# Performance work log

Hardware: AMD Instinct MI355X
Metric: run time of the kernel (lower is better)

## Reference

```python
import jax, jax.numpy as jnp
import numpy as np


def setup_inputs() -> dict:
    key = jax.random.key(0)
    k1, k2 = jax.random.split(key)
    x = jax.random.normal(k1, (32, 3, 512, 512), dtype=jnp.float32)
    p = jax.random.uniform(k2, (32, 4), dtype=jnp.float32)
    return {"x": x, "p": p}


def _reflect(coord, size):
    # PyTorch grid_sample reflection padding, align_corners=False:
    # reflect about borders at -0.5 and size-0.5 (span = size), then clip.
    span = float(size)
    c = jnp.abs(coord + 0.5)
    flips = jnp.floor(c / span)
    extra = c - flips * span
    c = jnp.where(jnp.mod(flips, 2.0) == 0.0, extra, span - extra) - 0.5
    return jnp.clip(c, 0.0, size - 1.0)


def _bilinear_sample(img, ix, iy, W, H):
    # img: [C,H,W]; ix,iy: [H,W] pixel-space coords already reflected into [0,size-1]
    ix0f = jnp.floor(ix)
    iy0f = jnp.floor(iy)
    fx = ix - ix0f
    fy = iy - iy0f
    x0 = jnp.clip(ix0f.astype(jnp.int32), 0, W - 1)
    x1 = jnp.clip(ix0f.astype(jnp.int32) + 1, 0, W - 1)
    y0 = jnp.clip(iy0f.astype(jnp.int32), 0, H - 1)
    y1 = jnp.clip(iy0f.astype(jnp.int32) + 1, 0, H - 1)
    v00 = img[:, y0, x0]  # [C,H,W]
    v01 = img[:, y0, x1]
    v10 = img[:, y1, x0]
    v11 = img[:, y1, x1]
    return (v00 * (1.0 - fx) * (1.0 - fy)
            + v01 * fx * (1.0 - fy)
            + v10 * (1.0 - fx) * fy
            + v11 * fx * fy)


def reference(x, p):
    B, C, H, W = x.shape
    tx, ty, th, ts = p[:, 0], p[:, 1], p[:, 2], p[:, 3]
    c, s = jnp.cos(th), jnp.sin(th)
    # affine_grid base coords, align_corners=False: centers of pixels in [-1,1]
    xs = (jnp.arange(W, dtype=x.dtype) + 0.5) * (2.0 / W) - 1.0  # [W]
    ys = (jnp.arange(H, dtype=x.dtype) + 0.5) * (2.0 / H) - 1.0  # [H]
    a = (ts * c)[:, None, None]
    b = (-ts * s)[:, None, None]
    d = (ts * s)[:, None, None]
    e = (ts * c)[:, None, None]
    gx = a * xs[None, None, :] + b * ys[None, :, None] + tx[:, None, None]  # [B,H,W]
    gy = d * xs[None, None, :] + e * ys[None, :, None] + ty[:, None, None]  # [B,H,W]
    # unnormalize to pixel space (align_corners=False)
    ix = ((gx + 1.0) * W - 1.0) * 0.5
    iy = ((gy + 1.0) * H - 1.0) * 0.5
    ix = _reflect(ix, W)
    iy = _reflect(iy, H)
    out = jax.vmap(lambda img, jx, jy: _bilinear_sample(img, jx, jy, W, H))(x, ix, iy)
    return out
```

## Files before the change

kernel.cpp:

```cpp
#include <hip/hip_runtime.h>


#define B_ 32
#define C_ 3
#define H_ 512
#define W_ 512
#define TILE 32
#define LSTRIDE 60
#define MAXROWS 55
#define SMEMW (MAXROWS * LSTRIDE + 64)

typedef float f32x4 __attribute__((ext_vector_type(4)));

__device__ __forceinline__ float reflect512(float coord) {
    const float c = fabsf(coord + 0.5f);
    const float m = c - floorf(c * (1.0f / 1024.0f)) * 1024.0f;
    const float t = 512.0f - fabsf(m - 512.0f);
    return fminf(fmaxf(t - 0.5f, 0.0f), 511.0f);
}

__global__ __launch_bounds__(256, 8)
void st_kernel(const float* __restrict__ x, const float* __restrict__ p,
               float* __restrict__ out) {
    __shared__ float smem[SMEMW];

    const int tid = threadIdx.x;

    const int bid = blockIdx.x;
    const int wid = (bid & 7) * 1024 + (bid >> 3);
    const int b   = wid >> 8;
    const int til = wid & 255;
    const int tlx = til & 15;
    const int tly = til >> 4;

    const float tx = p[b * 4 + 0];
    const float ty = p[b * 4 + 1];
    const float th = p[b * 4 + 2];
    const float ts = p[b * 4 + 3];
    const float cth = __cosf(th), sth = __sinf(th);
    const float a  =  ts * cth;
    const float bb = -ts * sth;
    const float d  =  ts * sth;

    const float xs_c = ((float)(tlx * TILE) + 16.0f) * (2.0f / W_) - 1.0f;
    const float ys_c = ((float)(tly * TILE) + 16.0f) * (2.0f / H_) - 1.0f;
    const float gxc = a * xs_c + bb * ys_c + tx;
    const float gyc = d * xs_c + a  * ys_c + ty;
    const float rcx = reflect512(((gxc + 1.0f) * W_ - 1.0f) * 0.5f);
    const float rcy = reflect512(((gyc + 1.0f) * H_ - 1.0f) * 0.5f);
    const float ext = 16.0f * (fabsf(a) + fabsf(bb)) + 3.0f;

    int bx0 = max((int)floorf(rcx - ext), 0) & ~3;
    const int xhi = min((int)ceilf(rcx + ext) + 1, W_);
    int nw4 = (xhi - bx0 + 3) >> 2;
    nw4 = min(min(nw4, 15), (W_ - bx0) >> 2);

    int by0 = max((int)floorf(rcy - ext), 0);
    const int yhi = min((int)ceilf(rcy + ext) + 1, H_);
    const int nrows = min(yhi - by0, MAXROWS);

    const size_t plane = (size_t)H_ * W_;
    const float* img = x + (size_t)b * C_ * plane;
    const int c4 = tid & 15;
    const int r0 = tid >> 4;
    const int ccl = min(c4, max(nw4 - 1, 0)) * 4;
    const float* gp0 = img + (size_t)by0 * W_ + bx0;

    f32x4 vr[4];
    #pragma unroll
    for (int i = 0; i < 4; ++i) {
        const int rr = min(r0 + i * 16, nrows - 1);
        vr[i] = *reinterpret_cast<const f32x4*>(gp0 + (size_t)rr * W_ + ccl);
    }

    const int lr   = tid >> 3;
    const int lc   = (tid & 7) * 4;
    const int row  = tly * TILE + lr;
    const int col0 = tlx * TILE + lc;

    const float ysn = ((float)row  + 0.5f) * (2.0f / H_) - 1.0f;
    const float xsn = ((float)col0 + 0.5f) * (2.0f / W_) - 1.0f;
    float ix = ((a * xsn + bb * ysn + tx + 1.0f) * W_ - 1.0f) * 0.5f;
    float iy = ((d * xsn + a  * ysn + ty + 1.0f) * H_ - 1.0f) * 0.5f;

    const int koff = by0 * LSTRIDE + bx0;
    int   idx4[4];
    float fx_[4], fy_[4];
    #pragma unroll
    for (int k = 0; k < 4; ++k) {
        const float rx  = reflect512(ix);
        const float ry  = reflect512(iy);
        const float x0f = floorf(rx);
        const float y0f = floorf(ry);
        fx_[k] = rx - x0f;
        fy_[k] = ry - y0f;
        idx4[k] = (int)y0f * LSTRIDE + (int)x0f - koff;
        ix += a;
        iy += d;
    }

    #pragma unroll
    for (int i = 0; i < 4; ++i) {
        const int r = r0 + i * 16;
        if (r < nrows && c4 < nw4)
            *reinterpret_cast<f32x4*>(&smem[r * LSTRIDE + c4 * 4]) = vr[i];
    }
    if (nw4 < 15) {
        #pragma unroll
        for (int i = 0; i < 4; ++i) {
            const int r = r0 + i * 16;
            if (r < nrows && c4 == nw4)
                *reinterpret_cast<f32x4*>(&smem[r * LSTRIDE + c4 * 4]) = (f32x4)(0.0f);
        }
    }
    if (tid < 16)
        *reinterpret_cast<f32x4*>(&smem[nrows * LSTRIDE + tid * 4]) = (f32x4)(0.0f);

    float* outp = out + (size_t)b * C_ * plane + (size_t)row * W_ + col0;

    #pragma unroll
    for (int ch = 0; ch < C_; ++ch) {
        __syncthreads();

        float acc[4];
        #pragma unroll
        for (int k = 0; k < 4; ++k) {
            const float fx = fx_[k], fy = fy_[k];
            const float ox = 1.0f - fx, oy = 1.0f - fy;
            const float* s = &smem[idx4[k]];
            acc[k] = s[0] * (ox * oy) + s[1] * (fx * oy)
                   + s[LSTRIDE] * (ox * fy) + s[LSTRIDE + 1] * (fx * fy);
        }
        const f32x4 v = {acc[0], acc[1], acc[2], acc[3]};
        *reinterpret_cast<f32x4*>(outp + (size_t)ch * plane) = v;

        if (ch < C_ - 1) {
            const float* gp = img + (size_t)(ch + 1) * plane
                                  + (size_t)by0 * W_ + bx0;
            #pragma unroll
            for (int i = 0; i < 4; ++i) {
                const int rr = min(r0 + i * 16, nrows - 1);
                vr[i] = *reinterpret_cast<const f32x4*>(gp + (size_t)rr * W_ + ccl);
            }
            __syncthreads();
            #pragma unroll
            for (int i = 0; i < 4; ++i) {
                const int r = r0 + i * 16;
                if (r < nrows && c4 < nw4)
                    *reinterpret_cast<f32x4*>(&smem[r * LSTRIDE + c4 * 4]) = vr[i];
            }
        }
    }
}

extern "C" void kernel_launch(void* const* d_in, const int* in_sizes, int n_in,
                              void* d_out, int out_size, void* d_ws, size_t ws_size,
                              hipStream_t stream) {
    const float* x = (const float*)d_in[0];
    const float* p = (const float*)d_in[1];
    float* out = (float*)d_out;

    dim3 block(256, 1, 1);
    dim3 grid((W_ / TILE) * (H_ / TILE) * B_, 1, 1);
    st_kernel<<<grid, block, 0, stream>>>(x, p, out);
}
```

Before: 179.7 us.

## Give each wavefront its own 16x16 sub-tile window and drop block barriers

Splits the 32x32 output tile into four 16x16 sub-tiles, one per wavefront, each staging its own smaller source window in a private LDS region. Because only one wavefront reads and writes its window, all __syncthreads calls are removed, and the next channel's global loads are issued before the current channel's interpolation so they overlap with compute. The cost is more overlapping halo loads across wavefronts, more registers for eight prefetched vectors, and reliance on wavefront lockstep for LDS ordering with no explicit barrier. Large rotations or scales may exceed the smaller window and get clamped.

```diff
diff --git a/kernel.cpp b/kernel.cpp
--- a/kernel.cpp
+++ b/kernel.cpp
@@ -6,9 +6,10 @@
 #define H_ 512
 #define W_ 512
 #define TILE 32
-#define LSTRIDE 60
-#define MAXROWS 55
-#define SMEMW (MAXROWS * LSTRIDE + 64)
+#define PTILE 16
+#define LSTRIDE 40
+#define WROWS 32
+#define WWORDS (WROWS * LSTRIDE)
 
 typedef float f32x4 __attribute__((ext_vector_type(4)));
 
@@ -22,9 +23,11 @@
 __global__ __launch_bounds__(256, 8)
 void st_kernel(const float* __restrict__ x, const float* __restrict__ p,
                float* __restrict__ out) {
-    __shared__ float smem[SMEMW];
+    __shared__ float smem[4 * WWORDS];
 
-    const int tid = threadIdx.x;
+    const int tid  = threadIdx.x;
+    const int wv   = tid >> 6;
+    const int lane = tid & 63;
 
     const int bid = blockIdx.x;
     const int wid = (bid & 7) * 1024 + (bid >> 3);
@@ -42,41 +45,59 @@
     const float bb = -ts * sth;
     const float d  =  ts * sth;
 
-    const float xs_c = ((float)(tlx * TILE) + 16.0f) * (2.0f / W_) - 1.0f;
-    const float ys_c = ((float)(tly * TILE) + 16.0f) * (2.0f / H_) - 1.0f;
+    const int porow = tly * TILE + (wv >> 1) * PTILE;
+    const int pocol = tlx * TILE + (wv & 1) * PTILE;
+
+    const float xs_c = ((float)pocol + 8.0f) * (2.0f / W_) - 1.0f;
+    const float ys_c = ((float)porow + 8.0f) * (2.0f / H_) - 1.0f;
     const float gxc = a * xs_c + bb * ys_c + tx;
     const float gyc = d * xs_c + a  * ys_c + ty;
     const float rcx = reflect512(((gxc + 1.0f) * W_ - 1.0f) * 0.5f);
     const float rcy = reflect512(((gyc + 1.0f) * H_ - 1.0f) * 0.5f);
-    const float ext = 16.0f * (fabsf(a) + fabsf(bb)) + 3.0f;
+    const float ext = 8.0f * (fabsf(a) + fabsf(bb)) + 3.0f;
 
     int bx0 = max((int)floorf(rcx - ext), 0) & ~3;
     const int xhi = min((int)ceilf(rcx + ext) + 1, W_);
     int nw4 = (xhi - bx0 + 3) >> 2;
-    nw4 = min(min(nw4, 15), (W_ - bx0) >> 2);
+    nw4 = min(min(nw4, 9), (W_ - bx0) >> 2);
 
     int by0 = max((int)floorf(rcy - ext), 0);
     const int yhi = min((int)ceilf(rcy + ext) + 1, H_);
-    const int nrows = min(yhi - by0, MAXROWS);
+    const int nrows = min(yhi - by0, WROWS - 1);
 
     const size_t plane = (size_t)H_ * W_;
     const float* img = x + (size_t)b * C_ * plane;
-    const int c4 = tid & 15;
-    const int r0 = tid >> 4;
-    const int ccl = min(c4, max(nw4 - 1, 0)) * 4;
-    const float* gp0 = img + (size_t)by0 * W_ + bx0;
+    const size_t goff = (size_t)by0 * W_ + bx0;
 
-    f32x4 vr[4];
-    #pragma unroll
-    for (int i = 0; i < 4; ++i) {
-        const int rr = min(r0 + i * 16, nrows - 1);
-        vr[i] = *reinterpret_cast<const f32x4*>(gp0 + (size_t)rr * W_ + ccl);
-    }
+    float* wbase = &smem[wv * WWORDS];
+    const int slot = lane & 15;
+    const int r0   = lane >> 4;
+    const int ccl  = min(slot, max(nw4 - 1, 0)) * 4;
 
-    const int lr   = tid >> 3;
-    const int lc   = (tid & 7) * 4;
-    const int row  = tly * TILE + lr;
-    const int col0 = tlx * TILE + lc;
+    f32x4 vr[8];
+    auto load_ch = [&](int ch) {
+        const float* gp = img + (size_t)ch * plane + goff;
+        #pragma unroll
+        for (int i = 0; i < 8; ++i) {
+            const int rr = min(r0 + 4 * i, nrows - 1);
+            vr[i] = *reinterpret_cast<const f32x4*>(gp + (size_t)rr * W_ + ccl);
+        }
+    };
+    auto write_ch = [&]() {
+        #pragma unroll
+        for (int i = 0; i < 8; ++i) {
+            const int r = r0 + 4 * i;
+            if (r < nrows && slot < nw4)
+                *reinterpret_cast<f32x4*>(wbase + r * LSTRIDE + slot * 4) = vr[i];
+        }
+    };
+
+    load_ch(0);
+
+    const int lrow = lane >> 2;
+    const int lcol = (lane & 3) * 4;
+    const int row  = porow + lrow;
+    const int col0 = pocol + lcol;
 
     const float ysn = ((float)row  + 0.5f) * (2.0f / H_) - 1.0f;
     const float xsn = ((float)col0 + 0.5f) * (2.0f / W_) - 1.0f;
@@ -99,57 +120,39 @@
         iy += d;
     }
 
-    #pragma unroll
-    for (int i = 0; i < 4; ++i) {
-        const int r = r0 + i * 16;
-        if (r < nrows && c4 < nw4)
-            *reinterpret_cast<f32x4*>(&smem[r * LSTRIDE + c4 * 4]) = vr[i];
-    }
-    if (nw4 < 15) {
+    if (slot == nw4) {
         #pragma unroll
-        for (int i = 0; i < 4; ++i) {
-            const int r = r0 + i * 16;
-            if (r < nrows && c4 == nw4)
-                *reinterpret_cast<f32x4*>(&smem[r * LSTRIDE + c4 * 4]) = (f32x4)(0.0f);
+        for (int i = 0; i < 8; ++i) {
+            const int r = r0 + 4 * i;
+            if (r < nrows)
+                *reinterpret_cast<f32x4*>(wbase + r * LSTRIDE + slot * 4) = (f32x4)(0.0f);
         }
     }
-    if (tid < 16)
-        *reinterpret_cast<f32x4*>(&smem[nrows * LSTRIDE + tid * 4]) = (f32x4)(0.0f);
+    if (lane < 10)
+        *reinterpret_cast<f32x4*>(wbase + nrows * LSTRIDE + lane * 4) = (f32x4)(0.0f);
+
+    write_ch();
 
     float* outp = out + (size_t)b * C_ * plane + (size_t)row * W_ + col0;
 
     #pragma unroll
     for (int ch = 0; ch < C_; ++ch) {
-        __syncthreads();
-
+        if (ch < C_ - 1)
+            load_ch(ch + 1);
         float acc[4];
         #pragma unroll
         for (int k = 0; k < 4; ++k) {
             const float fx = fx_[k], fy = fy_[k];
             const float ox = 1.0f - fx, oy = 1.0f - fy;
-            const float* s = &smem[idx4[k]];
+            const float* s = wbase + idx4[k];
             acc[k] = s[0] * (ox * oy) + s[1] * (fx * oy)
                    + s[LSTRIDE] * (ox * fy) + s[LSTRIDE + 1] * (fx * fy);
         }
         const f32x4 v = {acc[0], acc[1], acc[2], acc[3]};
         *reinterpret_cast<f32x4*>(outp + (size_t)ch * plane) = v;
 
-        if (ch < C_ - 1) {
-            const float* gp = img + (size_t)(ch + 1) * plane
-                                  + (size_t)by0 * W_ + bx0;
-            #pragma unroll
-            for (int i = 0; i < 4; ++i) {
-                const int rr = min(r0 + i * 16, nrows - 1);
-                vr[i] = *reinterpret_cast<const f32x4*>(gp + (size_t)rr * W_ + ccl);
-            }
-            __syncthreads();
-            #pragma unroll
-            for (int i = 0; i < 4; ++i) {
-                const int r = r0 + i * 16;
-                if (r < nrows && c4 < nw4)
-                    *reinterpret_cast<f32x4*>(&smem[r * LSTRIDE + c4 * 4]) = vr[i];
-            }
-        }
+        if (ch < C_ - 1)
+            write_ch();
     }
 }
 
```

Measured after the change: 262.5 us. +46.0%, slower.
